# Kernel optimization log

Hardware: AMD Instinct MI355X
Metric: run time of the kernel (lower is better)

Reference implementation:

```python
import jax, jax.numpy as jnp
import numpy as np

LN_EPS = 1e-5   # torch LayerNorm default
NRM_EPS = 1e-8  # normalizer-state epsilon in mLSTMCell


def setup_inputs() -> dict:
    key = jax.random.key(0)
    ks = jax.random.split(key, 3)
    B, T, H, L, O = 32, 256, 1024, 4, 256
    x = jax.random.normal(ks[0], (B, T, H), dtype=jnp.float32)
    # 6 projections per layer in order (q, k, v, i, f, o); Linear stored as [in, out]
    W = jax.random.normal(ks[1], (L, 6, H, H), dtype=jnp.float32) * 0.02
    b = jnp.zeros((L, 6, H), dtype=jnp.float32)
    ln_g = jnp.ones((L, 6, H), dtype=jnp.float32)
    ln_b = jnp.zeros((L, 6, H), dtype=jnp.float32)
    fc_w = jax.random.normal(ks[2], (H, O), dtype=jnp.float32) * 0.02
    fc_b = jnp.zeros((O,), dtype=jnp.float32)
    return {"x": x, "W": W, "b": b, "ln_g": ln_g, "ln_b": ln_b,
            "fc_w": fc_w, "fc_b": fc_b}


def _layer_norm(z, g, beta):
    # z: [6, B, H]; g, beta: [6, H]
    mu = z.mean(-1, keepdims=True)
    var = z.var(-1, keepdims=True)
    return (z - mu) * jax.lax.rsqrt(var + LN_EPS) * g[:, None, :] + beta[:, None, :]


def _cell(x_in, h_prev, c_prev, n_prev, Wl, bl, gl, betal):
    # x_in: [B, H]; states: [B, H]; Wl: [6, H, H]
    z = jnp.einsum('bh,jhd->jbd', x_in, Wl) + bl[:, None, :]
    z = _layer_norm(z, gl, betal)
    q, k, v, zi, zf, zo = z  # q is computed by the original cell but unused
    i = jnp.exp(zi)
    f = jax.nn.sigmoid(zf)
    o = jax.nn.sigmoid(zo)
    # kv_interaction = outer(k, v); sum over dim=1 == sum(k) * v (same math, no [B,H,H])
    kv_sum = k.sum(-1, keepdims=True) * v
    c = f * c_prev + i * kv_sum
    n = f * n_prev + i * k
    n_hat = n / (jnp.linalg.norm(n, axis=-1, keepdims=True) + NRM_EPS)
    h = o * jnp.tanh(c * n_hat)
    return h, c, n


def _mlstm_forward(x, W, b, ln_g, ln_b, fc_w, fc_b):
    B, T, H = x.shape
    L = W.shape[0]
    h0 = jnp.zeros((L, B, H), x.dtype)
    init = (h0, h0, h0)  # (h, c, n)

    def step(carry, x_t):
        h, c, n = carry
        layer_in = x_t
        hs, cs, ns = [], [], []
        for l in range(L):  # small fixed layer count
            h_l, c_l, n_l = _cell(layer_in, h[l], c[l], n[l],
                                  W[l], b[l], ln_g[l], ln_b[l])
            if l > 0:  # residual connection (use_residual=True)
                h_l = h_l + layer_in
            layer_in = h_l
            hs.append(h_l); cs.append(c_l); ns.append(n_l)
        return (jnp.stack(hs), jnp.stack(cs), jnp.stack(ns)), None

    (h, c, n), _ = jax.lax.scan(step, init, jnp.swapaxes(x, 0, 1))
    # output[-1] == top-layer hidden at the final timestep
    out = h[-1] @ fc_w + fc_b  # [B, O]
    return out, (h, c, n)


def reference(x, W, b, ln_g, ln_b, fc_w, fc_b):
    return _mlstm_forward(x, W, b, ln_g, ln_b, fc_w, fc_b)
```

## Files before the change

kernel.cpp:

```cpp
#include <hip/hip_runtime.h>
#include <hip/hip_bf16.h>
#include <math.h>

#define H 1024
#define B 32
#define T 256
#define L 4
#define O 256
#define SEGLEN 16
#define NSEG (T / SEGLEN)

typedef _Float16 half8 __attribute__((ext_vector_type(8)));
typedef _Float16 half4 __attribute__((ext_vector_type(4)));
typedef float f32x4 __attribute__((ext_vector_type(4)));

#define X_PK_OFF   0
#define HB0_OFF    8388608
#define HB1_OFF    16777216
#define WT2_OFF    25165824
#define Z16_OFF    46137344
#define A_OFF      88080384
#define BC_OFF     104857600
#define BN_OFF     121634816
#define STATS_OFF  138412032
#define CARC_OFF   138608640
#define CARN_OFF   139657216
#define STATE_OFF  140705792
#define FCP_OFF    141230080

__global__ __launch_bounds__(256) void pack_w(const float* __restrict__ W,
                                              _Float16* __restrict__ Wt2) {
  int tile = blockIdx.x;
  int m_idx = tile >> 8;
  int kt = (tile >> 4) & 15, ntt = tile & 15;
  int l = m_idx / 5, jj = m_idx % 5;
  const float* Wf = W + ((size_t)(l * 6 + jj + 1) << 20);
  _Float16* out = Wt2 + ((size_t)m_idx << 20);
  __shared__ float ts[64][65];
  int k0 = kt * 64, n0 = ntt * 64;
#pragma unroll
  for (int s = 0; s < 16; ++s) {
    int e = threadIdx.x + s * 256;
    int kk = e >> 6, col = e & 63;
    ts[kk][col] = Wf[(size_t)(k0 + kk) * H + n0 + col];
  }
  __syncthreads();
#pragma unroll
  for (int gi = 0; gi < 2; ++gi) {
    int g = threadIdx.x * 2 + gi;
    int l64 = g & 63, ksl = (g >> 6) & 1, ntl = g >> 7;
    int nn = l64 & 15, kh = l64 >> 4;
    half8 tmp;
#pragma unroll
    for (int e = 0; e < 8; ++e)
      tmp[e] = (_Float16)ts[ksl * 32 + kh * 8 + e][ntl * 16 + nn];
    *(half8*)&out[(size_t)((ntt * 4 + ntl) * 32 + kt * 2 + ksl) * 512 + (size_t)l64 * 8] = tmp;
  }
}

__global__ __launch_bounds__(256) void pack_x(const float* __restrict__ x,
                                              _Float16* __restrict__ x_pk) {
  int t = blockIdx.x;
  __shared__ float ld[32][257];
  for (int c = 0; c < 4; ++c) {
#pragma unroll
    for (int s = 0; s < 32; ++s) {
      int e2 = threadIdx.x + s * 256;
      int b = e2 >> 8, col = e2 & 255;
      ld[b][col] = x[((size_t)b * T + t) * H + c * 256 + col];
    }
    __syncthreads();
#pragma unroll
    for (int s3 = 0; s3 < 4; ++s3) {
      int gg = threadIdx.x * 4 + s3;
      int l64 = gg & 63, ksl = (gg >> 6) & 7, bt = gg >> 9;
      int nn = l64 & 15, kh = l64 >> 4;
      int b = bt * 16 + nn;
      half8 tmp;
#pragma unroll
      for (int e = 0; e < 8; ++e)
        tmp[e] = (_Float16)ld[b][ksl * 32 + kh * 8 + e];
      *(half8*)&x_pk[(size_t)t * 32768 + (size_t)bt * 16384 +
                     (size_t)(c * 8 + ksl) * 512 + (size_t)l64 * 8] = tmp;
    }
    __syncthreads();
  }
}

__global__ __launch_bounds__(512) void gemm_big(
    const _Float16* __restrict__ A_pk, const _Float16* __restrict__ Wl,
    _Float16* __restrict__ z16) {
  int raw = blockIdx.x;
  int xcd = raw & 7, c = raw >> 3;
  int bm = (xcd >> 1) * 16 + (c & 15);
  int bn = (xcd & 1) * 10 + (c >> 4);
  int w = threadIdx.x >> 6, lane = threadIdx.x & 63;
  int wm = w >> 2, wn = w & 3;

  __shared__ _Float16 smem[24576];

  int j = bn >> 2;
  const _Float16* gsrc[3];
  int ldst[3];
#pragma unroll
  for (int q = 0; q < 3; ++q) {
    int f = w * 3 + q;
    if (f < 8) {
      gsrc[q] = A_pk + (size_t)(bm * 8 + f) * 16384 + lane * 8;
      ldst[q] = f * 512 + lane * 8;
    } else {
      int nf = f - 8;
      gsrc[q] = Wl + ((size_t)j << 20) + (size_t)((bn & 3) * 16 + nf) * 16384 + lane * 8;
      ldst[q] = 4096 + nf * 512 + lane * 8;
    }
  }

  half8 stA[3], stB[3];
#pragma unroll
  for (int q = 0; q < 3; ++q) stA[q] = *(const half8*)(gsrc[q]);
#pragma unroll
  for (int q = 0; q < 3; ++q) *(half8*)&smem[ldst[q]] = stA[q];
#pragma unroll
  for (int q = 0; q < 3; ++q) stA[q] = *(const half8*)(gsrc[q] + 512);
  __syncthreads();

  f32x4 acc[4][4] = {};
  int ardo = wm * 2048 + lane * 8;
  int brdo = 4096 + wn * 2048 + lane * 8;

  for (int ks = 0; ks < 32; ks += 2) {
    {
      if (ks + 2 < 32) {
#pragma unroll
        for (int q = 0; q < 3; ++q)
          stB[q] = *(const half8*)(gsrc[q] + (size_t)(ks + 2) * 512);
      }
      half8 a[4], b[4];
#pragma unroll
      for (int i = 0; i < 4; ++i) a[i] = *(const half8*)&smem[ardo + i * 512];
#pragma unroll
      for (int i = 0; i < 4; ++i) b[i] = *(const half8*)&smem[brdo + i * 512];
#pragma unroll
      for (int i = 0; i < 4; ++i)
#pragma unroll
        for (int jf = 0; jf < 4; ++jf)
          acc[i][jf] = __builtin_amdgcn_mfma_f32_16x16x32_f16(a[i], b[jf], acc[i][jf], 0, 0, 0);
#pragma unroll
      for (int q = 0; q < 3; ++q) *(half8*)&smem[12288 + ldst[q]] = stA[q];
      asm volatile("s_waitcnt lgkmcnt(0)" ::: "memory");
      __builtin_amdgcn_s_barrier();
      __builtin_amdgcn_sched_barrier(0);
    }
    {
      if (ks + 3 < 32) {
#pragma unroll
        for (int q = 0; q < 3; ++q)
          stA[q] = *(const half8*)(gsrc[q] + (size_t)(ks + 3) * 512);
      }
      half8 a[4], b[4];
#pragma unroll
      for (int i = 0; i < 4; ++i) a[i] = *(const half8*)&smem[12288 + ardo + i * 512];
#pragma unroll
      for (int i = 0; i < 4; ++i) b[i] = *(const half8*)&smem[12288 + brdo + i * 512];
#pragma unroll
      for (int i = 0; i < 4; ++i)
#pragma unroll
        for (int jf = 0; jf < 4; ++jf)
          acc[i][jf] = __builtin_amdgcn_mfma_f32_16x16x32_f16(a[i], b[jf], acc[i][jf], 0, 0, 0);
      if (ks + 2 < 32) {
#pragma unroll
        for (int q = 0; q < 3; ++q) *(half8*)&smem[ldst[q]] = stB[q];
        asm volatile("s_waitcnt lgkmcnt(0)" ::: "memory");
        __builtin_amdgcn_s_barrier();
        __builtin_amdgcn_sched_barrier(0);
      }
    }
  }
  __syncthreads();

  _Float16 (*cz)[264] = (_Float16(*)[264])smem;
  int hb0 = (bn & 3) * 256;
  for (int p = 0; p < 2; ++p) {
    if (p) __syncthreads();
    if (wm == p) {
#pragma unroll
      for (int i = 0; i < 4; ++i)
#pragma unroll
        for (int jf = 0; jf < 4; ++jf)
#pragma unroll
          for (int r = 0; r < 4; ++r)
            cz[i * 16 + (lane >> 4) * 4 + r][wn * 64 + jf * 16 + (lane & 15)] =
                (_Float16)acc[i][jf][r];
    }
    __syncthreads();
#pragma unroll
    for (int s = 0; s < 4; ++s) {
      int e = threadIdx.x + s * 512;
      int r = e >> 5, h8 = e & 31;
      int m_local = bm * 128 + p * 64 + r;
      half8 vv = *(const half8*)&cz[r][h8 * 8];
      *(half8*)&z16[((size_t)m_local * 5 + j) * 1024 + hb0 + h8 * 8] = vv;
    }
  }
}

__global__ __launch_bounds__(256) void stats_kernel(
    const _Float16* __restrict__ z16, const float* __restrict__ bias,
    const float* __restrict__ ln_g, const float* __restrict__ ln_b,
    float* __restrict__ stats, int l) {
  int row = blockIdx.x, tid = threadIdx.x;
  int h0 = tid * 4;
  float red[13];
#pragma unroll
  for (int jj = 0; jj < 5; ++jj) {
    half4 z4 = *(const half4*)&z16[((size_t)row * 5 + jj) * 1024 + h0];
    float4 bb = *(const float4*)&bias[(size_t)(l * 6 + 1 + jj) * H + h0];
    float vx = (float)z4[0] + bb.x, vy = (float)z4[1] + bb.y,
          vz = (float)z4[2] + bb.z, vw = (float)z4[3] + bb.w;
    red[jj * 2] = vx + vy + vz + vw;
    red[jj * 2 + 1] = vx * vx + vy * vy + vz * vz + vw * vw;
    if (jj == 0) {
      float4 g = *(const float4*)&ln_g[(size_t)(l * 6 + 1) * H + h0];
      float4 be = *(const float4*)&ln_b[(size_t)(l * 6 + 1) * H + h0];
      red[10] = vx * g.x + vy * g.y + vz * g.z + vw * g.w;
      red[11] = g.x + g.y + g.z + g.w;
      red[12] = be.x + be.y + be.z + be.w;
    }
  }
#pragma unroll
  for (int off = 32; off; off >>= 1)
#pragma unroll
    for (int q = 0; q < 13; ++q) red[q] += __shfl_down(red[q], off);
  __shared__ float sb[4][13];
  if ((tid & 63) == 0) {
#pragma unroll
    for (int q = 0; q < 13; ++q) sb[tid >> 6][q] = red[q];
  }
  __syncthreads();
  if (tid == 0) {
    float st[13];
#pragma unroll
    for (int q = 0; q < 13; ++q) st[q] = sb[0][q] + sb[1][q] + sb[2][q] + sb[3][q];
    float* so = stats + (size_t)row * 12;
#pragma unroll
    for (int jj = 0; jj < 5; ++jj) {
      float mu = st[jj * 2] * (1.0f / H);
      float var = st[jj * 2 + 1] * (1.0f / H) - mu * mu;
      so[jj * 2] = mu;
      so[jj * 2 + 1] = rsqrtf(var + 1e-5f);
    }
    float mu0 = st[0] * (1.0f / H);
    float rs0 = rsqrtf(st[1] * (1.0f / H) - mu0 * mu0 + 1e-5f);
    so[10] = rs0 * (st[10] - mu0 * st[11]) + st[12];
    so[11] = 0.f;
  }
}

__global__ __launch_bounds__(256) void scan_p1(
    const _Float16* __restrict__ z16, const float* __restrict__ stats,
    const float* __restrict__ bias, const float* __restrict__ ln_g,
    const float* __restrict__ ln_b, float* __restrict__ Abuf,
    float* __restrict__ Bc, float* __restrict__ Bn, int l) {
  int idx = blockIdx.x * 256 + threadIdx.x;
  int h = idx & 1023;
  int bs = idx >> 10;
  int b = bs & 31, seg = bs >> 5;

  float bz[4], gg[4], bb[4];
#pragma unroll
  for (int jj = 0; jj < 4; ++jj) {
    bz[jj] = bias[(size_t)(l * 6 + 1 + jj) * H + h];
    gg[jj] = ln_g[(size_t)(l * 6 + 1 + jj) * H + h];
    bb[jj] = ln_b[(size_t)(l * 6 + 1 + jj) * H + h];
  }
  float A = 1.f, bc = 0.f, bn = 0.f;
#pragma unroll 2
  for (int u = 0; u < SEGLEN; ++u) {
    int row = (seg * SEGLEN + u) * 32 + b;
    size_t zb = ((size_t)row * 5) * 1024 + h;
    float zk = (float)z16[zb];
    float zv = (float)z16[zb + 1024];
    float zi = (float)z16[zb + 2048];
    float zf = (float)z16[zb + 3072];
    const float* st = stats + (size_t)row * 12;
    float k   = (zk + bz[0] - st[0]) * st[1] * gg[0] + bb[0];
    float v   = (zv + bz[1] - st[2]) * st[3] * gg[1] + bb[1];
    float zi_ = (zi + bz[2] - st[4]) * st[5] * gg[2] + bb[2];
    float zf_ = (zf + bz[3] - st[6]) * st[7] * gg[3] + bb[3];
    float iv = __expf(zi_);
    float fv = 1.f / (1.f + __expf(-zf_));
    A *= fv;
    bn = fv * bn + iv * k;
    bc = fv * bc + iv * (st[10] * v);
    size_t o = (size_t)row * 1024 + h;
    Abuf[o] = A;
    Bn[o] = bn;
    Bc[o] = bc;
  }
}

__global__ __launch_bounds__(256) void scan_p2(
    const float* __restrict__ Abuf, const float* __restrict__ Bc,
    const float* __restrict__ Bn, float* __restrict__ carC,
    float* __restrict__ carN) {
  int idx = blockIdx.x * 256 + threadIdx.x;
  int h = idx & 1023, b = idx >> 10;
  float cc = 0.f, nn = 0.f;
#pragma unroll
  for (int seg = 0; seg < NSEG; ++seg) {
    size_t coff = (size_t)seg * 32768 + (size_t)b * 1024 + h;
    carC[coff] = cc;
    carN[coff] = nn;
    int rowLast = (seg * SEGLEN + SEGLEN - 1) * 32 + b;
    size_t o = (size_t)rowLast * 1024 + h;
    float a = Abuf[o];
    cc = Bc[o] + a * cc;
    nn = Bn[o] + a * nn;
  }
}

__global__ __launch_bounds__(256) void final_kernel(
    const _Float16* __restrict__ z16, const float* __restrict__ stats,
    const float* __restrict__ bias, const float* __restrict__ ln_g,
    const float* __restrict__ ln_b, const float* __restrict__ Abuf,
    const float* __restrict__ Bc, const float* __restrict__ Bn,
    const float* __restrict__ carC, const float* __restrict__ carN,
    const _Float16* __restrict__ hin, _Float16* __restrict__ hout,
    float* __restrict__ out, int l) {
  int row = blockIdx.x;
  int b = row & 31, t = row >> 5, seg = t / SEGLEN;
  int tid = threadIdx.x, h0 = tid * 4;
  size_t o = (size_t)row * 1024 + h0;
  size_t coff = (size_t)seg * 32768 + (size_t)b * 1024 + h0;
  float4 a4 = *(const float4*)&Abuf[o];
  float4 bn4 = *(const float4*)&Bn[o];
  float4 bc4 = *(const float4*)&Bc[o];
  float4 cN = *(const float4*)&carN[coff];
  float4 cC = *(const float4*)&carC[coff];
  float nn[4] = {bn4.x + a4.x * cN.x, bn4.y + a4.y * cN.y,
                 bn4.z + a4.z * cN.z, bn4.w + a4.w * cN.w};
  float cc[4] = {bc4.x + a4.x * cC.x, bc4.y + a4.y * cC.y,
                 bc4.z + a4.z * cC.z, bc4.w + a4.w * cC.w};

  float ss = nn[0] * nn[0] + nn[1] * nn[1] + nn[2] * nn[2] + nn[3] * nn[3];
#pragma unroll
  for (int off = 32; off; off >>= 1) ss += __shfl_down(ss, off);
  __shared__ float sb[4];
  if ((tid & 63) == 0) sb[tid >> 6] = ss;
  __syncthreads();
  float rn = 1.f / (sqrtf(sb[0] + sb[1] + sb[2] + sb[3]) + 1e-8f);

  half4 zo4 = *(const half4*)&z16[((size_t)row * 5 + 4) * 1024 + h0];
  const float* st = stats + (size_t)row * 12;
  float mu = st[8], rs = st[9];
  float4 bz = *(const float4*)&bias[(size_t)(l * 6 + 5) * H + h0];
  float4 g4 = *(const float4*)&ln_g[(size_t)(l * 6 + 5) * H + h0];
  float4 be4 = *(const float4*)&ln_b[(size_t)(l * 6 + 5) * H + h0];
  float gv[4] = {g4.x, g4.y, g4.z, g4.w};
  float bev[4] = {be4.x, be4.y, be4.z, be4.w};
  float zov[4] = {(float)zo4[0] + bz.x, (float)zo4[1] + bz.y,
                  (float)zo4[2] + bz.z, (float)zo4[3] + bz.w};

  size_t hfoff = (size_t)(b >> 4) * 16384 + (size_t)(h0 >> 5) * 512 +
                 (size_t)((((h0 & 31) >> 3) * 16) + (b & 15)) * 8 + (h0 & 7);
  half4 rin;
  if (l > 0) rin = *(const half4*)&hin[(size_t)t * 32768 + hfoff];

  float hh[4];
#pragma unroll
  for (int u = 0; u < 4; ++u) {
    float ov = 1.f / (1.f + __expf(-((zov[u] - mu) * rs * gv[u] + bev[u])));
    float targ = cc[u] * (nn[u] * rn);
    float e2 = __expf(-2.f * fabsf(targ));
    float th = copysignf((1.f - e2) / (1.f + e2), targ);
    hh[u] = ov * th + ((l > 0) ? (float)rin[u] : 0.f);
  }
  half4 hx;
  hx[0] = (_Float16)hh[0]; hx[1] = (_Float16)hh[1];
  hx[2] = (_Float16)hh[2]; hx[3] = (_Float16)hh[3];
  *(half4*)&hout[(size_t)t * 32768 + hfoff] = hx;

  if (t == T - 1) {
    *(float4*)&out[8192 + (size_t)l * 32768 + (size_t)b * 1024 + h0] =
        make_float4(hh[0], hh[1], hh[2], hh[3]);
    *(float4*)&out[8192 + 131072 + ((size_t)(l * B) + b) * 1024 + h0] =
        make_float4(cc[0], cc[1], cc[2], cc[3]);
    *(float4*)&out[8192 + 262144 + ((size_t)(l * B) + b) * 1024 + h0] =
        make_float4(nn[0], nn[1], nn[2], nn[3]);
  }
}

__global__ __launch_bounds__(256) void fc_part(
    const float* __restrict__ out_h, const float* __restrict__ fc_w,
    float* __restrict__ partial) {
  int b = blockIdx.x >> 3, kh = blockIdx.x & 7;
  int o = threadIdx.x;
  const float* hr = out_h + (size_t)b * 1024 + kh * 128;
  const float* wp = fc_w + (size_t)kh * 128 * O + o;
  float acc = 0.f;
#pragma unroll 8
  for (int h = 0; h < 128; ++h)
    acc = fmaf(hr[h], wp[(size_t)h * O], acc);
  partial[((size_t)kh * 32 + b) * O + o] = acc;
}

__global__ __launch_bounds__(256) void fc_reduce(
    const float* __restrict__ partial, const float* __restrict__ fc_b,
    float* __restrict__ out) {
  int b = blockIdx.x, o = threadIdx.x;
  float acc = fc_b[o];
#pragma unroll
  for (int kh = 0; kh < 8; ++kh)
    acc += partial[((size_t)kh * 32 + b) * O + o];
  out[(size_t)b * O + o] = acc;
}

extern "C" void kernel_launch(void* const* d_in, const int* in_sizes, int n_in,
                              void* d_out, int out_size, void* d_ws, size_t ws_size,
                              hipStream_t stream) {
  const float* x    = (const float*)d_in[0];
  const float* W    = (const float*)d_in[1];
  const float* bias = (const float*)d_in[2];
  const float* ln_g = (const float*)d_in[3];
  const float* ln_b = (const float*)d_in[4];
  const float* fc_w = (const float*)d_in[5];
  const float* fc_b = (const float*)d_in[6];
  float* out = (float*)d_out;
  _Float16* wsh = (_Float16*)d_ws;

  _Float16* x_pk = wsh + X_PK_OFF;
  _Float16* hb[2] = {wsh + HB0_OFF, wsh + HB1_OFF};
  _Float16* Wt2  = wsh + WT2_OFF;
  _Float16* z16  = wsh + Z16_OFF;
  float* Abuf  = (float*)(wsh + A_OFF);
  float* Bc    = (float*)(wsh + BC_OFF);
  float* Bn    = (float*)(wsh + BN_OFF);
  float* stats = (float*)(wsh + STATS_OFF);
  float* carC  = (float*)(wsh + CARC_OFF);
  float* carN  = (float*)(wsh + CARN_OFF);
  float* fcp   = (float*)(wsh + FCP_OFF);

  pack_w<<<5120, 256, 0, stream>>>(W, Wt2);
  pack_x<<<256, 256, 0, stream>>>(x, x_pk);

  for (int l = 0; l < L; ++l) {
    const _Float16* A_in = (l == 0) ? x_pk : hb[(l - 1) & 1];
    _Float16* h_out = hb[l & 1];
    const _Float16* Wl = Wt2 + ((size_t)(l * 5) << 20);
    gemm_big<<<1280, 512, 0, stream>>>(A_in, Wl, z16);
    stats_kernel<<<8192, 256, 0, stream>>>(z16, bias, ln_g, ln_b, stats, l);
    scan_p1<<<2048, 256, 0, stream>>>(z16, stats, bias, ln_g, ln_b,
                                      Abuf, Bc, Bn, l);
    scan_p2<<<128, 256, 0, stream>>>(Abuf, Bc, Bn, carC, carN);
    final_kernel<<<8192, 256, 0, stream>>>(z16, stats, bias, ln_g, ln_b,
                                           Abuf, Bc, Bn, carC, carN,
                                           A_in, h_out, out, l);
  }
  fc_part<<<256, 256, 0, stream>>>(out + 8192 + 3 * 32768, fc_w, fcp);
  fc_reduce<<<B, 256, 0, stream>>>(fcp, fc_b, out);
}
```

Before: 793.6 us.

## Recompute intra-segment scan in final kernel instead of storing per-step prefix buffers

The first scan pass now stores only per-segment aggregates (A, Bc, Bn) rather than full per-timestep prefix arrays. The final kernel reruns the recurrence within each segment, starting from the carried-in state, recomputing the gates from z16 and the stats. This removes large fp32 buffer writes and reads each layer. In exchange it re-reads z16, duplicates the gate math, and runs far fewer blocks with a per-step block barrier, which could reduce latency hiding.

New measurement: 753.7 us. 1.05x faster.

```diff
diff --git a/kernel.cpp b/kernel.cpp
--- a/kernel.cpp
+++ b/kernel.cpp
@@ -19,14 +19,13 @@
 #define HB1_OFF    16777216
 #define WT2_OFF    25165824
 #define Z16_OFF    46137344
-#define A_OFF      88080384
-#define BC_OFF     104857600
-#define BN_OFF     121634816
-#define STATS_OFF  138412032
-#define CARC_OFF   138608640
-#define CARN_OFF   139657216
-#define STATE_OFF  140705792
-#define FCP_OFF    141230080
+#define SEGA_OFF   88080384
+#define SEGBC_OFF  89128960
+#define SEGBN_OFF  90177536
+#define STATS_OFF  91226112
+#define CARC_OFF   91422720
+#define CARN_OFF   92471296
+#define FCP_OFF    93519872
 
 __global__ __launch_bounds__(256) void pack_w(const float* __restrict__ W,
                                               _Float16* __restrict__ Wt2) {
@@ -256,11 +255,11 @@
   }
 }
 
-__global__ __launch_bounds__(256) void scan_p1(
+__global__ __launch_bounds__(256) void scan_p1agg(
     const _Float16* __restrict__ z16, const float* __restrict__ stats,
     const float* __restrict__ bias, const float* __restrict__ ln_g,
-    const float* __restrict__ ln_b, float* __restrict__ Abuf,
-    float* __restrict__ Bc, float* __restrict__ Bn, int l) {
+    const float* __restrict__ ln_b, float* __restrict__ segA,
+    float* __restrict__ segBc, float* __restrict__ segBn, int l) {
   int idx = blockIdx.x * 256 + threadIdx.x;
   int h = idx & 1023;
   int bs = idx >> 10;
@@ -292,16 +291,16 @@
     A *= fv;
     bn = fv * bn + iv * k;
     bc = fv * bc + iv * (st[10] * v);
-    size_t o = (size_t)row * 1024 + h;
-    Abuf[o] = A;
-    Bn[o] = bn;
-    Bc[o] = bc;
-  }
+  }
+  size_t so = ((size_t)seg * 32 + b) * 1024 + h;
+  segA[so] = A;
+  segBn[so] = bn;
+  segBc[so] = bc;
 }
 
 __global__ __launch_bounds__(256) void scan_p2(
-    const float* __restrict__ Abuf, const float* __restrict__ Bc,
-    const float* __restrict__ Bn, float* __restrict__ carC,
+    const float* __restrict__ segA, const float* __restrict__ segBc,
+    const float* __restrict__ segBn, float* __restrict__ carC,
     float* __restrict__ carN) {
   int idx = blockIdx.x * 256 + threadIdx.x;
   int h = idx & 1023, b = idx >> 10;
@@ -311,82 +310,114 @@
     size_t coff = (size_t)seg * 32768 + (size_t)b * 1024 + h;
     carC[coff] = cc;
     carN[coff] = nn;
-    int rowLast = (seg * SEGLEN + SEGLEN - 1) * 32 + b;
-    size_t o = (size_t)rowLast * 1024 + h;
-    float a = Abuf[o];
-    cc = Bc[o] + a * cc;
-    nn = Bn[o] + a * nn;
-  }
-}
-
-__global__ __launch_bounds__(256) void final_kernel(
+    size_t so = ((size_t)seg * 32 + b) * 1024 + h;
+    float a = segA[so];
+    cc = segBc[so] + a * cc;
+    nn = segBn[so] + a * nn;
+  }
+}
+
+__global__ __launch_bounds__(256) void final_scan(
     const _Float16* __restrict__ z16, const float* __restrict__ stats,
     const float* __restrict__ bias, const float* __restrict__ ln_g,
-    const float* __restrict__ ln_b, const float* __restrict__ Abuf,
-    const float* __restrict__ Bc, const float* __restrict__ Bn,
-    const float* __restrict__ carC, const float* __restrict__ carN,
-    const _Float16* __restrict__ hin, _Float16* __restrict__ hout,
-    float* __restrict__ out, int l) {
-  int row = blockIdx.x;
-  int b = row & 31, t = row >> 5, seg = t / SEGLEN;
+    const float* __restrict__ ln_b, const float* __restrict__ carC,
+    const float* __restrict__ carN, const _Float16* __restrict__ hin,
+    _Float16* __restrict__ hout, float* __restrict__ out, int l) {
+  int seg = blockIdx.x >> 5, b = blockIdx.x & 31;
   int tid = threadIdx.x, h0 = tid * 4;
-  size_t o = (size_t)row * 1024 + h0;
+
+  float bz[5][4], gg[5][4], bb[5][4];
+#pragma unroll
+  for (int jj = 0; jj < 5; ++jj) {
+    float4 t1 = *(const float4*)&bias[(size_t)(l * 6 + 1 + jj) * H + h0];
+    float4 t2 = *(const float4*)&ln_g[(size_t)(l * 6 + 1 + jj) * H + h0];
+    float4 t3 = *(const float4*)&ln_b[(size_t)(l * 6 + 1 + jj) * H + h0];
+    bz[jj][0] = t1.x; bz[jj][1] = t1.y; bz[jj][2] = t1.z; bz[jj][3] = t1.w;
+    gg[jj][0] = t2.x; gg[jj][1] = t2.y; gg[jj][2] = t2.z; gg[jj][3] = t2.w;
+    bb[jj][0] = t3.x; bb[jj][1] = t3.y; bb[jj][2] = t3.z; bb[jj][3] = t3.w;
+  }
+
   size_t coff = (size_t)seg * 32768 + (size_t)b * 1024 + h0;
-  float4 a4 = *(const float4*)&Abuf[o];
-  float4 bn4 = *(const float4*)&Bn[o];
-  float4 bc4 = *(const float4*)&Bc[o];
-  float4 cN = *(const float4*)&carN[coff];
-  float4 cC = *(const float4*)&carC[coff];
-  float nn[4] = {bn4.x + a4.x * cN.x, bn4.y + a4.y * cN.y,
-                 bn4.z + a4.z * cN.z, bn4.w + a4.w * cN.w};
-  float cc[4] = {bc4.x + a4.x * cC.x, bc4.y + a4.y * cC.y,
-                 bc4.z + a4.z * cC.z, bc4.w + a4.w * cC.w};
-
-  float ss = nn[0] * nn[0] + nn[1] * nn[1] + nn[2] * nn[2] + nn[3] * nn[3];
-#pragma unroll
-  for (int off = 32; off; off >>= 1) ss += __shfl_down(ss, off);
-  __shared__ float sb[4];
-  if ((tid & 63) == 0) sb[tid >> 6] = ss;
-  __syncthreads();
-  float rn = 1.f / (sqrtf(sb[0] + sb[1] + sb[2] + sb[3]) + 1e-8f);
-
-  half4 zo4 = *(const half4*)&z16[((size_t)row * 5 + 4) * 1024 + h0];
-  const float* st = stats + (size_t)row * 12;
-  float mu = st[8], rs = st[9];
-  float4 bz = *(const float4*)&bias[(size_t)(l * 6 + 5) * H + h0];
-  float4 g4 = *(const float4*)&ln_g[(size_t)(l * 6 + 5) * H + h0];
-  float4 be4 = *(const float4*)&ln_b[(size_t)(l * 6 + 5) * H + h0];
-  float gv[4] = {g4.x, g4.y, g4.z, g4.w};
-  float bev[4] = {be4.x, be4.y, be4.z, be4.w};
-  float zov[4] = {(float)zo4[0] + bz.x, (float)zo4[1] + bz.y,
-                  (float)zo4[2] + bz.z, (float)zo4[3] + bz.w};
+  float4 cC4 = *(const float4*)&carC[coff];
+  float4 cN4 = *(const float4*)&carN[coff];
+  float c_[4] = {cC4.x, cC4.y, cC4.z, cC4.w};
+  float n_[4] = {cN4.x, cN4.y, cN4.z, cN4.w};
 
   size_t hfoff = (size_t)(b >> 4) * 16384 + (size_t)(h0 >> 5) * 512 +
                  (size_t)((((h0 & 31) >> 3) * 16) + (b & 15)) * 8 + (h0 & 7);
-  half4 rin;
-  if (l > 0) rin = *(const half4*)&hin[(size_t)t * 32768 + hfoff];
-
-  float hh[4];
-#pragma unroll
-  for (int u = 0; u < 4; ++u) {
-    float ov = 1.f / (1.f + __expf(-((zov[u] - mu) * rs * gv[u] + bev[u])));
-    float targ = cc[u] * (nn[u] * rn);
-    float e2 = __expf(-2.f * fabsf(targ));
-    float th = copysignf((1.f - e2) / (1.f + e2), targ);
-    hh[u] = ov * th + ((l > 0) ? (float)rin[u] : 0.f);
-  }
-  half4 hx;
-  hx[0] = (_Float16)hh[0]; hx[1] = (_Float16)hh[1];
-  hx[2] = (_Float16)hh[2]; hx[3] = (_Float16)hh[3];
-  *(half4*)&hout[(size_t)t * 32768 + hfoff] = hx;
-
-  if (t == T - 1) {
-    *(float4*)&out[8192 + (size_t)l * 32768 + (size_t)b * 1024 + h0] =
-        make_float4(hh[0], hh[1], hh[2], hh[3]);
-    *(float4*)&out[8192 + 131072 + ((size_t)(l * B) + b) * 1024 + h0] =
-        make_float4(cc[0], cc[1], cc[2], cc[3]);
-    *(float4*)&out[8192 + 262144 + ((size_t)(l * B) + b) * 1024 + h0] =
-        make_float4(nn[0], nn[1], nn[2], nn[3]);
+  __shared__ float sbuf[2][4];
+
+  half4 zr[5];
+  {
+    int row0 = (seg * SEGLEN) * 32 + b;
+#pragma unroll
+    for (int jj = 0; jj < 5; ++jj)
+      zr[jj] = *(const half4*)&z16[((size_t)row0 * 5 + jj) * 1024 + h0];
+  }
+
+  for (int u = 0; u < SEGLEN; ++u) {
+    int t = seg * SEGLEN + u;
+    int row = t * 32 + b;
+    half4 zc[5];
+#pragma unroll
+    for (int jj = 0; jj < 5; ++jj) zc[jj] = zr[jj];
+    if (u + 1 < SEGLEN) {
+      int rown = (t + 1) * 32 + b;
+#pragma unroll
+      for (int jj = 0; jj < 5; ++jj)
+        zr[jj] = *(const half4*)&z16[((size_t)rown * 5 + jj) * 1024 + h0];
+    }
+    half4 rin;
+    if (l > 0) rin = *(const half4*)&hin[(size_t)t * 32768 + hfoff];
+
+    const float* st = stats + (size_t)row * 12;
+    float mu0 = st[0], rs0 = st[1], mu1 = st[2], rs1 = st[3];
+    float mu2 = st[4], rs2 = st[5], mu3 = st[6], rs3 = st[7];
+    float mu4 = st[8], rs4 = st[9], ksum = st[10];
+
+    float ss = 0.f;
+#pragma unroll
+    for (int e = 0; e < 4; ++e) {
+      float k   = ((float)zc[0][e] + bz[0][e] - mu0) * rs0 * gg[0][e] + bb[0][e];
+      float v   = ((float)zc[1][e] + bz[1][e] - mu1) * rs1 * gg[1][e] + bb[1][e];
+      float zi_ = ((float)zc[2][e] + bz[2][e] - mu2) * rs2 * gg[2][e] + bb[2][e];
+      float zf_ = ((float)zc[3][e] + bz[3][e] - mu3) * rs3 * gg[3][e] + bb[3][e];
+      float iv = __expf(zi_);
+      float fv = 1.f / (1.f + __expf(-zf_));
+      n_[e] = fv * n_[e] + iv * k;
+      c_[e] = fv * c_[e] + iv * (ksum * v);
+      ss += n_[e] * n_[e];
+    }
+#pragma unroll
+    for (int off = 32; off; off >>= 1) ss += __shfl_down(ss, off);
+    if ((tid & 63) == 0) sbuf[u & 1][tid >> 6] = ss;
+    __syncthreads();
+    float nrm = sbuf[u & 1][0] + sbuf[u & 1][1] + sbuf[u & 1][2] + sbuf[u & 1][3];
+    float rn = 1.f / (sqrtf(nrm) + 1e-8f);
+
+    float hh[4];
+#pragma unroll
+    for (int e = 0; e < 4; ++e) {
+      float zo_ = ((float)zc[4][e] + bz[4][e] - mu4) * rs4 * gg[4][e] + bb[4][e];
+      float ov = 1.f / (1.f + __expf(-zo_));
+      float targ = c_[e] * (n_[e] * rn);
+      float e2 = __expf(-2.f * fabsf(targ));
+      float th = copysignf((1.f - e2) / (1.f + e2), targ);
+      hh[e] = ov * th + ((l > 0) ? (float)rin[e] : 0.f);
+    }
+    half4 hx;
+    hx[0] = (_Float16)hh[0]; hx[1] = (_Float16)hh[1];
+    hx[2] = (_Float16)hh[2]; hx[3] = (_Float16)hh[3];
+    *(half4*)&hout[(size_t)t * 32768 + hfoff] = hx;
+
+    if (t == T - 1) {
+      *(float4*)&out[8192 + (size_t)l * 32768 + (size_t)b * 1024 + h0] =
+          make_float4(hh[0], hh[1], hh[2], hh[3]);
+      *(float4*)&out[8192 + 131072 + ((size_t)(l * B) + b) * 1024 + h0] =
+          make_float4(c_[0], c_[1], c_[2], c_[3]);
+      *(float4*)&out[8192 + 262144 + ((size_t)(l * B) + b) * 1024 + h0] =
+          make_float4(n_[0], n_[1], n_[2], n_[3]);
+    }
   }
 }
 
@@ -432,9 +463,9 @@
   _Float16* hb[2] = {wsh + HB0_OFF, wsh + HB1_OFF};
   _Float16* Wt2  = wsh + WT2_OFF;
   _Float16* z16  = wsh + Z16_OFF;
-  float* Abuf  = (float*)(wsh + A_OFF);
-  float* Bc    = (float*)(wsh + BC_OFF);
-  float* Bn    = (float*)(wsh + BN_OFF);
+  float* segA  = (float*)(wsh + SEGA_OFF);
+  float* segBc = (float*)(wsh + SEGBC_OFF);
+  float* segBn = (float*)(wsh + SEGBN_OFF);
   float* stats = (float*)(wsh + STATS_OFF);
   float* carC  = (float*)(wsh + CARC_OFF);
   float* carN  = (float*)(wsh + CARN_OFF);
@@ -449,12 +480,11 @@
     const _Float16* Wl = Wt2 + ((size_t)(l * 5) << 20);
     gemm_big<<<1280, 512, 0, stream>>>(A_in, Wl, z16);
     stats_kernel<<<8192, 256, 0, stream>>>(z16, bias, ln_g, ln_b, stats, l);
-    scan_p1<<<2048, 256, 0, stream>>>(z16, stats, bias, ln_g, ln_b,
-                                      Abuf, Bc, Bn, l);
-    scan_p2<<<128, 256, 0, stream>>>(Abuf, Bc, Bn, carC, carN);
-    final_kernel<<<8192, 256, 0, stream>>>(z16, stats, bias, ln_g, ln_b,
-                                           Abuf, Bc, Bn, carC, carN,
-                                           A_in, h_out, out, l);
+    scan_p1agg<<<2048, 256, 0, stream>>>(z16, stats, bias, ln_g, ln_b,
+                                         segA, segBc, segBn, l);
+    scan_p2<<<128, 256, 0, stream>>>(segA, segBc, segBn, carC, carN);
+    final_scan<<<512, 256, 0, stream>>>(z16, stats, bias, ln_g, ln_b,
+                                        carC, carN, A_in, h_out, out, l);
   }
   fc_part<<<256, 256, 0, stream>>>(out + 8192 + 3 * 32768, fc_w, fcp);
   fc_reduce<<<B, 256, 0, stream>>>(fcp, fc_b, out);
```
